# Kernel optimization log

Hardware: AMD Instinct MI355X
Metric: run time of the kernel (lower is better)

## Reference

```python
import jax, jax.numpy as jnp
import numpy as np

B, S, D = 4, 1024, 1024
H, DH = 16, 64
F = 4 * D
EPS = 1e-6


def _ln(x, scale, bias, axes=-1):
    mean = jnp.mean(x, axis=axes, keepdims=True)
    var = jnp.var(x, axis=axes, keepdims=True)
    return (x - mean) * jax.lax.rsqrt(var + EPS) * scale + bias


def setup_inputs() -> dict:
    key = jax.random.key(0)
    ks = jax.random.split(key, 20)
    sd = 1.0 / np.sqrt(D)
    sf = 1.0 / np.sqrt(F)
    inp = {
        'x': jax.random.normal(ks[0], (B, S, D), jnp.float32),
        'z': jax.random.normal(ks[1], (B, S, D), jnp.float32),
        'ln1_s': jnp.ones((D,), jnp.float32),
        'ln1_b': jnp.zeros((D,), jnp.float32),
        'Wq': jax.random.normal(ks[2], (D, D), jnp.float32) * sd,
        'bq': jnp.zeros((D,), jnp.float32),
        'Wk': jax.random.normal(ks[3], (D, D), jnp.float32) * sd,
        'bk': jnp.zeros((D,), jnp.float32),
        'Wv': jax.random.normal(ks[4], (D, D), jnp.float32) * sd,
        'bv': jnp.zeros((D,), jnp.float32),
        'qn_s': jnp.ones((H, DH), jnp.float32),
        'qn_b': jnp.zeros((H, DH), jnp.float32),
        'kn_s': jnp.ones((H, DH), jnp.float32),
        'kn_b': jnp.zeros((H, DH), jnp.float32),
        'Wo': jax.random.normal(ks[5], (D, D), jnp.float32) * sd,
        'bo': jnp.zeros((D,), jnp.float32),
        'ln2_s': jnp.ones((D,), jnp.float32),
        'ln2_b': jnp.zeros((D,), jnp.float32),
        'W1': jax.random.normal(ks[6], (D, F), jnp.float32) * sd,
        'b1': jnp.zeros((F,), jnp.float32),
        'W2': jax.random.normal(ks[7], (D, F), jnp.float32) * sd,
        'b2': jnp.zeros((F,), jnp.float32),
        'W3': jax.random.normal(ks[8], (F, D), jnp.float32) * sf,
        'b3': jnp.zeros((D,), jnp.float32),
    }
    return inp


def reference(x, z, ln1_s, ln1_b, Wq, bq, Wk, bk, Wv, bv, qn_s, qn_b, kn_s, kn_b,
              Wo, bo, ln2_s, ln2_b, W1, b1, W2, b2, W3, b3):
    # z is unused by the original module body
    x_skip = x
    xn = _ln(x, ln1_s, ln1_b)
    q = (xn @ Wq + bq).reshape(B, S, H, DH)
    k = (xn @ Wk + bk).reshape(B, S, H, DH)
    v = (xn @ Wv + bv).reshape(B, S, H, DH)
    # QK-norm: flax LayerNorm(feature_axes=(-2,-1)) still reduces over axis -1,
    # but carries (H, DH)-shaped scale/bias
    q = _ln(q, qn_s, qn_b)
    k = _ln(k, kn_s, kn_b)
    attn = jnp.einsum('bqhd,bkhd->bhqk', q, k) / jnp.sqrt(jnp.asarray(DH, q.dtype))
    attn = jax.nn.softmax(attn, axis=-1)
    out = jnp.einsum('bhqk,bkhd->bqhd', attn, v).reshape(B, S, D)
    x = x_skip + out @ Wo + bo
    x_skip = x
    xn = _ln(x, ln2_s, ln2_b)
    x1 = xn @ W1 + b1
    x2 = xn @ W2 + b2
    h = x1 * jax.nn.gelu(x2, approximate=True)  # GeGLU
    x = x_skip + h @ W3 + b3
    return x
```

## Files before the change

kernel.cpp:

```cpp
#include <hip/hip_runtime.h>

typedef unsigned short u16;
typedef __bf16  bfrag  __attribute__((ext_vector_type(8)));
typedef float   f32x4  __attribute__((ext_vector_type(4)));
typedef u16     u16x8  __attribute__((ext_vector_type(8)));
typedef u16     u16x4  __attribute__((ext_vector_type(4)));

__device__ __forceinline__ float bf2f(u16 u) {
    unsigned v = ((unsigned)u) << 16;
    return __builtin_bit_cast(float, v);
}
__device__ __forceinline__ u16 f2bf(float f) {
    unsigned x = __builtin_bit_cast(unsigned, f);
    unsigned r = (x + 0x7fffu + ((x >> 16) & 1u)) >> 16;
    return (u16)r;
}
__device__ __forceinline__ void g2l16(const u16* g, u16* l) {
    __builtin_amdgcn_global_load_lds((__attribute__((address_space(1))) void*)g,
                                     (__attribute__((address_space(3))) void*)l, 16, 0, 0);
}
__device__ __forceinline__ float gelu_tanh(float x) {
    float c = 1.5957691216057308f * (x + 0.044715f * x * x * x);
    return x * __frcp_rn(1.0f + __expf(-c));
}

#define SW64(l)   (((((l) & 7) ^ (((l) >> 3) & 7))) * 8)
#define RS64(kk, quad, l15)  (((((kk) * 4 + (quad)) ^ ((l15) & 7))) * 8)

__global__ __launch_bounds__(256) void wtln(
        const float* __restrict__ Wq, const float* __restrict__ Wk,
        const float* __restrict__ Wv, const float* __restrict__ Wo,
        const float* __restrict__ W1, const float* __restrict__ W2,
        const float* __restrict__ W3,
        u16* __restrict__ WqkvT, u16* __restrict__ WoT,
        u16* __restrict__ W12T, u16* __restrict__ W3T,
        const float* __restrict__ x, const float* __restrict__ ln1_s,
        const float* __restrict__ ln1_b, u16* __restrict__ xn1) {
    __shared__ float tile[32][33];
    int blk = blockIdx.x;
    if (blk >= 16384) {
        int row = blk - 16384, t = threadIdx.x;
        float4 v = ((const float4*)(x + (size_t)row * 1024))[t];
        float sum = v.x + v.y + v.z + v.w;
        float sq  = v.x * v.x + v.y * v.y + v.z * v.z + v.w * v.w;
#pragma unroll
        for (int off = 1; off < 64; off <<= 1) {
            sum += __shfl_xor(sum, off);
            sq  += __shfl_xor(sq,  off);
        }
        float* s1 = &tile[0][0];
        float* s2 = &tile[0][8];
        int wave = t >> 6;
        if ((t & 63) == 0) { s1[wave] = sum; s2[wave] = sq; }
        __syncthreads();
        sum = s1[0] + s1[1] + s1[2] + s1[3];
        sq  = s2[0] + s2[1] + s2[2] + s2[3];
        float mean = sum * (1.0f / 1024.0f);
        float var  = sq  * (1.0f / 1024.0f) - mean * mean;
        float inv  = rsqrtf(var + 1e-6f);
        float4 sc = ((const float4*)ln1_s)[t], bb = ((const float4*)ln1_b)[t];
        u16x4 o;
        o[0] = f2bf((v.x - mean) * inv * sc.x + bb.x);
        o[1] = f2bf((v.y - mean) * inv * sc.y + bb.y);
        o[2] = f2bf((v.z - mean) * inv * sc.z + bb.z);
        o[3] = f2bf((v.w - mean) * inv * sc.w + bb.w);
        *(u16x4*)&xn1[(size_t)row * 1024 + t * 4] = o;
        return;
    }
    const float* W; u16* Wt; int R, C, local; int ilv = -1;
    if (blk < 3072) {
        int w = blk >> 10; local = blk & 1023;
        W = (w == 0) ? Wq : (w == 1) ? Wk : Wv;
        Wt = WqkvT + (size_t)w * 1024 * 1024; R = 1024; C = 1024;
    } else if (blk < 4096) { W = Wo; Wt = WoT; R = 1024; C = 1024; local = blk - 3072; }
    else if (blk < 8192)   { W = W1; Wt = W12T; R = 1024; C = 4096; local = blk - 4096; ilv = 0; }
    else if (blk < 12288)  { W = W2; Wt = W12T; R = 1024; C = 4096; local = blk - 8192; ilv = 1; }
    else                   { W = W3; Wt = W3T; R = 4096; C = 1024; local = blk - 12288; }
    int tiles_x = C >> 5;
    int c0 = (local % tiles_x) * 32, r0 = (local / tiles_x) * 32;
    int tx = threadIdx.x & 31, ty = threadIdx.x >> 5;
#pragma unroll
    for (int i = 0; i < 32; i += 8)
        tile[ty + i][tx] = W[(size_t)(r0 + ty + i) * C + c0 + tx];
    __syncthreads();
#pragma unroll
    for (int i = 0; i < 32; i += 8) {
        int c = c0 + ty + i;
        int orow = (ilv < 0) ? c : ((c >> 6) * 128 + ilv * 64 + (c & 63));
        Wt[(size_t)orow * R + r0 + tx] = f2bf(tile[tx][ty + i]);
    }
}

template <int EPI>
__global__ __launch_bounds__(256, 3) void gemm64(const u16* __restrict__ A,
                                                 const u16* __restrict__ Bt,
                                                 const float* __restrict__ bias,
                                                 const float* __restrict__ bias2,
                                                 const float* __restrict__ bias3,
                                                 const float* __restrict__ qn_s,
                                                 const float* __restrict__ qn_b,
                                                 const float* __restrict__ kn_s,
                                                 const float* __restrict__ kn_b,
                                                 u16* __restrict__ o0,
                                                 u16* __restrict__ o1,
                                                 u16* __restrict__ o2,
                                                 u16* __restrict__ o3,
                                                 int M, int N, int K, int Klen) {
    __shared__ u16 As[128 * 64];
    __shared__ u16 Bs[128 * 64];
    int tid = threadIdx.x, wave = tid >> 6, lane = tid & 63;
    int quad = lane >> 4, l15 = lane & 15;
    int row0 = blockIdx.y * 128, col0 = blockIdx.x * 128;
    int kz = blockIdx.z;
    int wr = (wave >> 1) * 64, wc = (wave & 1) * 64;
    int swz = SW64(lane);

    f32x4 acc[4][4] = {};

    const u16* gA = A  + (size_t)(row0 + wave * 32 + (lane >> 3)) * K + kz * Klen + swz;
    const u16* gB = Bt + (size_t)(col0 + wave * 32 + (lane >> 3)) * K + kz * Klen + swz;
    u16* lA = &As[wave * 32 * 64];
    u16* lB = &Bs[wave * 32 * 64];

    for (int k0 = 0; k0 < Klen; k0 += 64) {
        __syncthreads();
#pragma unroll
        for (int j = 0; j < 4; j++) {
            g2l16(gA + k0 + j * 8 * K, lA + j * 8 * 64);
            g2l16(gB + k0 + j * 8 * K, lB + j * 8 * 64);
        }
        __syncthreads();
#pragma unroll
        for (int kk = 0; kk < 2; kk++) {
            int rs = RS64(kk, quad, l15);
            bfrag af[4], bf[4];
#pragma unroll
            for (int mi = 0; mi < 4; mi++)
                af[mi] = *(const bfrag*)&As[(wr + mi * 16 + l15) * 64 + rs];
#pragma unroll
            for (int ni = 0; ni < 4; ni++)
                bf[ni] = *(const bfrag*)&Bs[(wc + ni * 16 + l15) * 64 + rs];
#pragma unroll
            for (int mi = 0; mi < 4; mi++)
#pragma unroll
                for (int ni = 0; ni < 4; ni++)
                    acc[mi][ni] = __builtin_amdgcn_mfma_f32_16x16x32_bf16(
                        af[mi], bf[ni], acc[mi][ni], 0, 0, 0);
        }
    }

    if (EPI == 0) {
        u16* P = (kz == 0) ? o0 : (kz == 1) ? o1 : (kz == 2) ? o2 : o3;
#pragma unroll
        for (int mi = 0; mi < 4; mi++) {
            int rbase = row0 + wr + mi * 16 + quad * 4;
#pragma unroll
            for (int r = 0; r < 4; r++)
#pragma unroll
                for (int ni = 0; ni < 4; ni++)
                    P[(size_t)(rbase + r) * N + col0 + wc + ni * 16 + l15] =
                        f2bf(acc[mi][ni][r]);
        }
    } else {
        int cbase = col0 + wc;
        int z = cbase >> 10;
        int hd = (cbase >> 6) & 15;
        const float* bp = (z == 0) ? bias : (z == 1) ? bias2 : bias3;
        float post = (z == 0) ? 0.125f : 1.0f;
        float bv[4], sn[4], bn[4];
#pragma unroll
        for (int ni = 0; ni < 4; ni++)
            bv[ni] = bp[(cbase & 1023) + ni * 16 + l15];
        if (z < 2) {
            const float* ns = (z == 0) ? qn_s : kn_s;
            const float* nb = (z == 0) ? qn_b : kn_b;
#pragma unroll
            for (int ni = 0; ni < 4; ni++) {
                sn[ni] = ns[hd * 64 + ni * 16 + l15];
                bn[ni] = nb[hd * 64 + ni * 16 + l15];
            }
        }
#pragma unroll
        for (int mi = 0; mi < 4; mi++) {
            int rbase = row0 + wr + mi * 16 + quad * 4;
#pragma unroll
            for (int r = 0; r < 4; r++) {
                float v0 = acc[mi][0][r] + bv[0];
                float v1 = acc[mi][1][r] + bv[1];
                float v2 = acc[mi][2][r] + bv[2];
                float v3 = acc[mi][3][r] + bv[3];
                size_t rb = (size_t)(rbase + r) * N + cbase;
                if (z == 2) {
                    o0[rb + 0 * 16 + l15] = f2bf(v0);
                    o0[rb + 1 * 16 + l15] = f2bf(v1);
                    o0[rb + 2 * 16 + l15] = f2bf(v2);
                    o0[rb + 3 * 16 + l15] = f2bf(v3);
                } else {
                    float s  = v0 + v1 + v2 + v3;
                    float sq = v0 * v0 + v1 * v1 + v2 * v2 + v3 * v3;
#pragma unroll
                    for (int m = 1; m < 16; m <<= 1) {
                        s  += __shfl_xor(s,  m);
                        sq += __shfl_xor(sq, m);
                    }
                    float mean = s * (1.0f / 64.0f);
                    float var  = sq * (1.0f / 64.0f) - mean * mean;
                    float inv  = rsqrtf(var + 1e-6f);
                    o0[rb + 0 * 16 + l15] = f2bf(((v0 - mean) * inv * sn[0] + bn[0]) * post);
                    o0[rb + 1 * 16 + l15] = f2bf(((v1 - mean) * inv * sn[1] + bn[1]) * post);
                    o0[rb + 2 * 16 + l15] = f2bf(((v2 - mean) * inv * sn[2] + bn[2]) * post);
                    o0[rb + 3 * 16 + l15] = f2bf(((v3 - mean) * inv * sn[3] + bn[3]) * post);
                }
            }
        }
    }
}

#define PH8(BUFI, S, ISSUE, TAIL)                                              \
  {                                                                            \
    const u16* LA = sm + (BUFI) * 32768;                                       \
    const u16* LB = LA + 16384;                                                \
    if ((S) == 0) {                                                            \
      _Pragma("unroll") for (int ni = 0; ni < 4; ++ni)                         \
      _Pragma("unroll") for (int kk = 0; kk < 2; ++kk)                         \
        bfr[ni][kk] = *(const bfrag*)&LB[(wcg + ni * 16 + l15) * 64            \
                                         + RS64(kk, quad, l15)];               \
    }                                                                          \
    bfrag a00 = *(const bfrag*)&LA[(wr128 + ((S)*2)     * 16 + l15) * 64 + RS64(0, quad, l15)]; \
    bfrag a01 = *(const bfrag*)&LA[(wr128 + ((S)*2)     * 16 + l15) * 64 + RS64(1, quad, l15)]; \
    bfrag a10 = *(const bfrag*)&LA[(wr128 + ((S)*2 + 1) * 16 + l15) * 64 + RS64(0, quad, l15)]; \
    bfrag a11 = *(const bfrag*)&LA[(wr128 + ((S)*2 + 1) * 16 + l15) * 64 + RS64(1, quad, l15)]; \
    ISSUE;                                                                     \
    asm volatile("" ::: "memory");                                             \
    __builtin_amdgcn_s_barrier();                                              \
    asm volatile("s_waitcnt lgkmcnt(0)" ::: "memory");                         \
    __builtin_amdgcn_s_setprio(1);                                             \
    _Pragma("unroll") for (int ni = 0; ni < 4; ++ni) {                         \
      acc[(S)*2][ni]     = __builtin_amdgcn_mfma_f32_16x16x32_bf16(a00, bfr[ni][0], acc[(S)*2][ni], 0, 0, 0);         \
      acc[(S)*2][ni]     = __builtin_amdgcn_mfma_f32_16x16x32_bf16(a01, bfr[ni][1], acc[(S)*2][ni], 0, 0, 0);         \
      acc[(S)*2 + 1][ni] = __builtin_amdgcn_mfma_f32_16x16x32_bf16(a10, bfr[ni][0], acc[(S)*2 + 1][ni], 0, 0, 0);     \
      acc[(S)*2 + 1][ni] = __builtin_amdgcn_mfma_f32_16x16x32_bf16(a11, bfr[ni][1], acc[(S)*2 + 1][ni], 0, 0, 0);     \
    }                                                                          \
    __builtin_amdgcn_s_setprio(0);                                             \
    TAIL;                                                                      \
    asm volatile("" ::: "memory");                                             \
    __builtin_amdgcn_s_barrier();                                              \
    asm volatile("" ::: "memory");                                             \
  }

__global__ __launch_bounds__(512, 2) void gemm_w12_8ph(
        const u16* __restrict__ A, const u16* __restrict__ BI,
        const float* __restrict__ b1, const float* __restrict__ b2,
        u16* __restrict__ H) {
    extern __shared__ __align__(16) u16 sm[];
    int tid = threadIdx.x, w = tid >> 6, lane = tid & 63;
    int quad = lane >> 4, l15 = lane & 15;
    int row0  = blockIdx.y * 256;
    int nrow0 = blockIdx.x * 256;
    int wr128 = (w >> 2) * 128, wcg = (w & 3) * 64;
    int strow = w * 8 + (lane >> 3);
    int swz8  = ((lane & 7) ^ ((lane >> 3) & 7)) * 8;
    int lw8   = w * 8;

    const u16* gA = A  + (size_t)(row0  + strow) * 1024 + swz8;
    const u16* gB = BI + (size_t)(nrow0 + strow) * 1024 + swz8;

    f32x4 acc[8][4] = {};
    bfrag bfr[4][2];

    auto stage = [&](int bufi, int isB, int half, int t) {
        const u16* g = (isB ? gB : gA) + (size_t)half * 128 * 1024 + t * 64;
        u16* l = sm + bufi * 32768 + isB * 16384 + (half * 128 + lw8) * 64;
        g2l16(g, l);
        g2l16(g + 64 * 1024, l + 64 * 64);
    };

    stage(0, 1, 0, 0); stage(0, 1, 1, 0);
    stage(0, 0, 0, 0); stage(0, 0, 1, 0);
    stage(1, 1, 0, 1); stage(1, 1, 1, 1);
    asm volatile("s_waitcnt vmcnt(4)" ::: "memory");
    __builtin_amdgcn_s_barrier();
    asm volatile("" ::: "memory");

#pragma unroll 1
    for (int i = 0; i < 8; ++i) {
        int t = 2 * i;
        bool more = (i < 7);
        PH8(0, 0, { stage(1, 0, 0, t + 1); }, {});
        PH8(0, 1, { stage(1, 0, 1, t + 1); }, {});
        PH8(0, 2, { if (more) stage(0, 1, 0, t + 2); }, {});
        PH8(0, 3, { if (more) stage(0, 1, 1, t + 2); },
                  { if (more) asm volatile("s_waitcnt vmcnt(4)" ::: "memory");
                    else      asm volatile("s_waitcnt vmcnt(0)" ::: "memory"); });
        PH8(1, 0, { if (more) stage(0, 0, 0, t + 2); }, {});
        PH8(1, 1, { if (more) stage(0, 0, 1, t + 2); }, {});
        PH8(1, 2, { if (more) stage(1, 1, 0, t + 3); }, {});
        PH8(1, 3, { if (more) stage(1, 1, 1, t + 3); },
                  { if (more) asm volatile("s_waitcnt vmcnt(4)" ::: "memory"); });
    }

    int c0 = blockIdx.x * 128 + ((w & 3) >> 1) * 64;
    const float* bp = (w & 1) ? b2 : b1;
    float bvv[4];
#pragma unroll
    for (int ni = 0; ni < 4; ++ni) bvv[ni] = bp[c0 + ni * 16 + l15];

    float* xg = (float*)(void*)sm + (w >> 1) * (128 * 64);
    if (w & 1) {
#pragma unroll
        for (int mi = 0; mi < 8; ++mi)
#pragma unroll
        for (int ni = 0; ni < 4; ++ni) {
            int lc = (ni * 16 + l15) ^ (quad << 4);
#pragma unroll
            for (int r = 0; r < 4; ++r)
                xg[(mi * 16 + quad * 4 + r) * 64 + lc] =
                    gelu_tanh(acc[mi][ni][r] + bvv[ni]);
        }
    }
    asm volatile("" ::: "memory");
    __builtin_amdgcn_s_barrier();
    asm volatile("" ::: "memory");
    if (!(w & 1)) {
#pragma unroll
        for (int mi = 0; mi < 8; ++mi) {
            int gr = row0 + wr128 + mi * 16 + quad * 4;
#pragma unroll
            for (int r = 0; r < 4; ++r)
#pragma unroll
            for (int ni = 0; ni < 4; ++ni) {
                float g = xg[(mi * 16 + quad * 4 + r) * 64
                             + ((ni * 16 + l15) ^ (quad << 4))];
                H[(size_t)(gr + r) * 4096 + c0 + ni * 16 + l15] =
                    f2bf((acc[mi][ni][r] + bvv[ni]) * g);
            }
        }
    }
}

__global__ __launch_bounds__(256) void reduce_ln(const u16* __restrict__ p0,
                                                 const u16* __restrict__ p1,
                                                 const float* __restrict__ x,
                                                 const float* __restrict__ bo,
                                                 const float* __restrict__ s,
                                                 const float* __restrict__ b,
                                                 float* __restrict__ xmid,
                                                 u16* __restrict__ xn2) {
    int row = blockIdx.x, t = threadIdx.x;
    size_t i = (size_t)row * 1024 + t * 4;
    float4 xv = *(const float4*)&x[i];
    float4 bb = *(const float4*)&bo[t * 4];
    u16x4 a0 = *(const u16x4*)&p0[i];
    u16x4 a1 = *(const u16x4*)&p1[i];
    float4 v;
    v.x = xv.x + bb.x + bf2f(a0[0]) + bf2f(a1[0]);
    v.y = xv.y + bb.y + bf2f(a0[1]) + bf2f(a1[1]);
    v.z = xv.z + bb.z + bf2f(a0[2]) + bf2f(a1[2]);
    v.w = xv.w + bb.w + bf2f(a0[3]) + bf2f(a1[3]);
    *(float4*)&xmid[i] = v;
    float sum = v.x + v.y + v.z + v.w;
    float sq  = v.x * v.x + v.y * v.y + v.z * v.z + v.w * v.w;
#pragma unroll
    for (int off = 1; off < 64; off <<= 1) {
        sum += __shfl_xor(sum, off);
        sq  += __shfl_xor(sq,  off);
    }
    __shared__ float s1[4], s2[4];
    int wave = t >> 6;
    if ((t & 63) == 0) { s1[wave] = sum; s2[wave] = sq; }
    __syncthreads();
    sum = s1[0] + s1[1] + s1[2] + s1[3];
    sq  = s2[0] + s2[1] + s2[2] + s2[3];
    float mean = sum * (1.0f / 1024.0f);
    float var  = sq  * (1.0f / 1024.0f) - mean * mean;
    float inv  = rsqrtf(var + 1e-6f);
    float4 sc = ((const float4*)s)[t], lb = ((const float4*)b)[t];
    u16x4 o;
    o[0] = f2bf((v.x - mean) * inv * sc.x + lb.x);
    o[1] = f2bf((v.y - mean) * inv * sc.y + lb.y);
    o[2] = f2bf((v.z - mean) * inv * sc.z + lb.z);
    o[3] = f2bf((v.w - mean) * inv * sc.w + lb.w);
    *(u16x4*)&xn2[i] = o;
}

__global__ __launch_bounds__(256) void reduce4(const u16* __restrict__ p0,
                                               const u16* __restrict__ p1,
                                               const u16* __restrict__ p2,
                                               const u16* __restrict__ p3,
                                               const float* __restrict__ xmid,
                                               const float* __restrict__ b3,
                                               float* __restrict__ out) {
    size_t i = ((size_t)blockIdx.x * 256 + threadIdx.x) * 4;
    float4 xm = *(const float4*)&xmid[i];
    float4 bb = *(const float4*)&b3[i & 1023];
    u16x4 a0 = *(const u16x4*)&p0[i];
    u16x4 a1 = *(const u16x4*)&p1[i];
    u16x4 a2 = *(const u16x4*)&p2[i];
    u16x4 a3 = *(const u16x4*)&p3[i];
    float4 o;
    o.x = xm.x + bb.x + bf2f(a0[0]) + bf2f(a1[0]) + bf2f(a2[0]) + bf2f(a3[0]);
    o.y = xm.y + bb.y + bf2f(a0[1]) + bf2f(a1[1]) + bf2f(a2[1]) + bf2f(a3[1]);
    o.z = xm.z + bb.z + bf2f(a0[2]) + bf2f(a1[2]) + bf2f(a2[2]) + bf2f(a3[2]);
    o.w = xm.w + bb.w + bf2f(a0[3]) + bf2f(a1[3]) + bf2f(a2[3]) + bf2f(a3[3]);
    *(float4*)&out[i] = o;
}

#define LPK 72
#define LPV 72
#define LPP 68
__global__ __launch_bounds__(256, 4) void flash(const u16* __restrict__ qkv,
                                                u16* __restrict__ o) {
    int qt = blockIdx.x, h = blockIdx.y, b = blockIdx.z;
    int tid = threadIdx.x, wave = tid >> 6, lane = tid & 63;
    int quad = lane >> 4, l15 = lane & 15;

    __shared__ u16 Ks[64 * LPK];
    __shared__ u16 Vt[64 * LPV];
    __shared__ u16 Ps[64 * LPP];

    const u16* qrow = qkv + (size_t)(b * 1024 + qt * 64 + wave * 16 + l15) * 3072
                      + h * 64 + quad * 8;
    bfrag aq0 = *(const bfrag*)qrow;
    bfrag aq1 = *(const bfrag*)(qrow + 32);

    f32x4 accO[4] = {};
    float l_run[4] = {0.f, 0.f, 0.f, 0.f};

    for (int kt = 0; kt < 16; kt++) {
        __syncthreads();
        {
            int row = tid >> 2, seg = tid & 3;
            const u16* ksrc = qkv + (size_t)(b * 1024 + kt * 64 + row) * 3072
                              + 1024 + h * 64 + seg * 16;
            *(u16x8*)&Ks[row * LPK + seg * 16]     = *(const u16x8*)ksrc;
            *(u16x8*)&Ks[row * LPK + seg * 16 + 8] = *(const u16x8*)(ksrc + 8);
        }
        {
            const u16* vsrc = qkv + (size_t)(b * 1024 + kt * 64 + lane) * 3072
                              + 2048 + h * 64 + wave * 16;
            u16x8 v0 = *(const u16x8*)vsrc, v1 = *(const u16x8*)(vsrc + 8);
#pragma unroll
            for (int j = 0; j < 8; j++) Vt[(wave * 16 + j) * LPV + lane]     = v0[j];
#pragma unroll
            for (int j = 0; j < 8; j++) Vt[(wave * 16 + 8 + j) * LPV + lane] = v1[j];
        }
        __syncthreads();

        f32x4 accS[4] = {};
#pragma unroll
        for (int ct = 0; ct < 4; ct++) {
            bfrag bk0 = *(const bfrag*)&Ks[(ct * 16 + l15) * LPK + quad * 8];
            bfrag bk1 = *(const bfrag*)&Ks[(ct * 16 + l15) * LPK + 32 + quad * 8];
            accS[ct] = __builtin_amdgcn_mfma_f32_16x16x32_bf16(aq0, bk0, accS[ct], 0, 0, 0);
            accS[ct] = __builtin_amdgcn_mfma_f32_16x16x32_bf16(aq1, bk1, accS[ct], 0, 0, 0);
        }

#pragma unroll
        for (int r = 0; r < 4; r++) {
            float p0 = __expf(accS[0][r]);
            float p1 = __expf(accS[1][r]);
            float p2 = __expf(accS[2][r]);
            float p3 = __expf(accS[3][r]);
            l_run[r] += (p0 + p1) + (p2 + p3);
            int pbase = (wave * 16 + quad * 4 + r) * LPP + l15;
            Ps[pbase + 0]  = f2bf(p0);
            Ps[pbase + 16] = f2bf(p1);
            Ps[pbase + 32] = f2bf(p2);
            Ps[pbase + 48] = f2bf(p3);
        }

#pragma unroll
        for (int kk = 0; kk < 2; kk++) {
            const u16* pp = &Ps[(wave * 16 + l15) * LPP + kk * 32 + quad * 8];
            u16x4 lo = *(const u16x4*)pp;
            u16x4 hi = *(const u16x4*)(pp + 4);
            u16x8 apu;
            apu[0] = lo[0]; apu[1] = lo[1]; apu[2] = lo[2]; apu[3] = lo[3];
            apu[4] = hi[0]; apu[5] = hi[1]; apu[6] = hi[2]; apu[7] = hi[3];
            bfrag ap = __builtin_bit_cast(bfrag, apu);
#pragma unroll
            for (int oc = 0; oc < 4; oc++) {
                bfrag bv = *(const bfrag*)&Vt[(oc * 16 + l15) * LPV + kk * 32 + quad * 8];
                accO[oc] = __builtin_amdgcn_mfma_f32_16x16x32_bf16(ap, bv, accO[oc], 0, 0, 0);
            }
        }
    }

#pragma unroll
    for (int r = 0; r < 4; r++) {
        float l = l_run[r];
#pragma unroll
        for (int m = 1; m < 16; m <<= 1) l += __shfl_xor(l, m);
        float linv = 1.0f / l;
        int srow = qt * 64 + wave * 16 + quad * 4 + r;
#pragma unroll
        for (int oc = 0; oc < 4; oc++)
            o[(size_t)(b * 1024 + srow) * 1024 + h * 64 + oc * 16 + l15] =
                f2bf(accO[oc][r] * linv);
    }
}

extern "C" void kernel_launch(void* const* d_in, const int* in_sizes, int n_in,
                              void* d_out, int out_size, void* d_ws, size_t ws_size,
                              hipStream_t stream) {
    const float* x     = (const float*)d_in[0];
    const float* ln1_s = (const float*)d_in[2];
    const float* ln1_b = (const float*)d_in[3];
    const float* Wq = (const float*)d_in[4];  const float* bq = (const float*)d_in[5];
    const float* Wk = (const float*)d_in[6];  const float* bk = (const float*)d_in[7];
    const float* Wv = (const float*)d_in[8];  const float* bv = (const float*)d_in[9];
    const float* qn_s = (const float*)d_in[10]; const float* qn_b = (const float*)d_in[11];
    const float* kn_s = (const float*)d_in[12]; const float* kn_b = (const float*)d_in[13];
    const float* Wo = (const float*)d_in[14]; const float* bo = (const float*)d_in[15];
    const float* ln2_s = (const float*)d_in[16]; const float* ln2_b = (const float*)d_in[17];
    const float* W1 = (const float*)d_in[18]; const float* b1 = (const float*)d_in[19];
    const float* W2 = (const float*)d_in[20]; const float* b2 = (const float*)d_in[21];
    const float* W3 = (const float*)d_in[22]; const float* b3 = (const float*)d_in[23];
    float* out = (float*)d_out;

    char* ws = (char*)d_ws;
    const size_t MB = (size_t)1 << 20;
    u16* WqkvT = (u16*)(ws + 0);
    u16* WoT   = (u16*)(ws + 6 * MB);
    u16* W12T  = (u16*)(ws + 8 * MB);
    u16* W3T   = (u16*)(ws + 24 * MB);
    u16* xn1   = (u16*)(ws + 32 * MB);
    u16* attn  = (u16*)(ws + 32 * MB);
    u16* xn2   = (u16*)(ws + 32 * MB);
    u16* qkv   = (u16*)(ws + 40 * MB);
    float* xmid = (float*)(ws + 40 * MB);
    u16* p3    = (u16*)(ws + 56 * MB);
    u16* h     = (u16*)(ws + 64 * MB);
    u16* wp0   = (u16*)(ws + 64 * MB);
    u16* wp1   = (u16*)(ws + 72 * MB);
    u16* p0    = (u16*)(ws + 0);
    u16* p1    = (u16*)(ws + 8 * MB);
    u16* p2    = (u16*)(ws + 16 * MB);

    wtln<<<20480, 256, 0, stream>>>(Wq, Wk, Wv, Wo, W1, W2, W3,
                                    WqkvT, WoT, W12T, W3T,
                                    x, ln1_s, ln1_b, xn1);

    gemm64<4><<<dim3(24, 32, 1), 256, 0, stream>>>(
        xn1, WqkvT, bq, bk, bv, qn_s, qn_b, kn_s, kn_b,
        qkv, nullptr, nullptr, nullptr, 4096, 3072, 1024, 1024);

    flash<<<dim3(16, 16, 4), 256, 0, stream>>>(qkv, attn);

    gemm64<0><<<dim3(8, 32, 2), 256, 0, stream>>>(
        attn, WoT, nullptr, nullptr, nullptr, nullptr, nullptr, nullptr, nullptr,
        wp0, wp1, nullptr, nullptr, 4096, 1024, 1024, 512);

    reduce_ln<<<4096, 256, 0, stream>>>(wp0, wp1, x, bo, ln2_s, ln2_b, xmid, xn2);

    gemm_w12_8ph<<<dim3(32, 16), 512, 131072, stream>>>(xn2, W12T, b1, b2, h);

    gemm64<0><<<dim3(8, 32, 4), 256, 0, stream>>>(
        h, W3T, nullptr, nullptr, nullptr, nullptr, nullptr, nullptr, nullptr,
        p0, p1, p2, p3, 4096, 1024, 4096, 1024);

    reduce4<<<4096, 256, 0, stream>>>(p0, p1, p2, p3, xmid, b3, out);
}
```

Measured before the change: 417.6 us.

## Remap W12 GEMM block order for XCD locality and split staging per phase

The W1/W2 GeGLU GEMM now launches as a 1D grid and remaps block ids so each group of consecutive blocks (one per XCD round-robin slot) covers neighbouring output tiles, aiming to improve L2 reuse of A and B panels. The global-to-LDS staging is reorganized so A rows for each wave come from its own compute quadrant and loads are issued in finer per-phase chunks, with waitcnts placed mid-iteration. This lets compute start on a partially loaded buffer and spreads memory issue more evenly across phases, but depends on the vmcnt accounting being exact.

```diff
diff --git a/kernel.cpp b/kernel.cpp
--- a/kernel.cpp
+++ b/kernel.cpp
@@ -215,6 +215,8 @@
         }
     }
 }
+
+#define VMC(n)  asm volatile("s_waitcnt vmcnt(" #n ")" ::: "memory")
 
 #define PH8(BUFI, S, ISSUE, TAIL)                                              \
   {                                                                            \
@@ -255,51 +257,62 @@
     extern __shared__ __align__(16) u16 sm[];
     int tid = threadIdx.x, w = tid >> 6, lane = tid & 63;
     int quad = lane >> 4, l15 = lane & 15;
-    int row0  = blockIdx.y * 256;
-    int nrow0 = blockIdx.x * 256;
+
+    int raw  = blockIdx.x;
+    int orig = (raw & 7) * 64 + (raw >> 3);
+    int bx = orig >> 4, by = orig & 15;
+    int row0  = by * 256;
+    int nrow0 = bx * 256;
+
     int wr128 = (w >> 2) * 128, wcg = (w & 3) * 64;
-    int strow = w * 8 + (lane >> 3);
     int swz8  = ((lane & 7) ^ ((lane >> 3) & 7)) * 8;
-    int lw8   = w * 8;
-
-    const u16* gA = A  + (size_t)(row0  + strow) * 1024 + swz8;
-    const u16* gB = BI + (size_t)(nrow0 + strow) * 1024 + swz8;
+
+    int rA = (w >> 2) * 128 + (w & 3) * 8 + (lane >> 3);
+    const u16* gA2 = A + (size_t)(row0 + rA) * 1024 + swz8;
+    int aRowW = (w >> 2) * 128 + (w & 3) * 8;
+    int rB = w * 8 + (lane >> 3);
+    const u16* gB2 = BI + (size_t)(nrow0 + rB) * 1024 + swz8;
+    int bRowW = w * 8;
 
     f32x4 acc[8][4] = {};
     bfrag bfr[4][2];
 
-    auto stage = [&](int bufi, int isB, int half, int t) {
-        const u16* g = (isB ? gB : gA) + (size_t)half * 128 * 1024 + t * 64;
-        u16* l = sm + bufi * 32768 + isB * 16384 + (half * 128 + lw8) * 64;
-        g2l16(g, l);
-        g2l16(g + 64 * 1024, l + 64 * 64);
+    auto stageA = [&](int bufi, int s, int t) {
+        g2l16(gA2 + (size_t)s * 32 * 1024 + t * 64,
+              sm + bufi * 32768 + (aRowW + s * 32) * 64);
     };
-
-    stage(0, 1, 0, 0); stage(0, 1, 1, 0);
-    stage(0, 0, 0, 0); stage(0, 0, 1, 0);
-    stage(1, 1, 0, 1); stage(1, 1, 1, 1);
-    asm volatile("s_waitcnt vmcnt(4)" ::: "memory");
+    auto stageB = [&](int bufi, int b, int t) {
+        g2l16(gB2 + (size_t)b * 64 * 1024 + t * 64,
+              sm + bufi * 32768 + 16384 + (bRowW + b * 64) * 64);
+    };
+
+    stageB(0, 0, 0); stageB(0, 1, 0); stageB(0, 2, 0); stageB(0, 3, 0);
+    stageA(0, 0, 0); stageA(0, 1, 0); stageA(0, 2, 0); stageA(0, 3, 0);
+    stageB(1, 0, 1); stageB(1, 1, 1); stageB(1, 2, 1); stageB(1, 3, 1);
+    stageA(1, 0, 1); stageA(1, 1, 1);
+    VMC(8);
     __builtin_amdgcn_s_barrier();
     asm volatile("" ::: "memory");
 
 #pragma unroll 1
     for (int i = 0; i < 8; ++i) {
-        int t = 2 * i;
+        int t1 = 2 * i + 1, t2 = 2 * i + 2, t3 = 2 * i + 3;
         bool more = (i < 7);
-        PH8(0, 0, { stage(1, 0, 0, t + 1); }, {});
-        PH8(0, 1, { stage(1, 0, 1, t + 1); }, {});
-        PH8(0, 2, { if (more) stage(0, 1, 0, t + 2); }, {});
-        PH8(0, 3, { if (more) stage(0, 1, 1, t + 2); },
-                  { if (more) asm volatile("s_waitcnt vmcnt(4)" ::: "memory");
-                    else      asm volatile("s_waitcnt vmcnt(0)" ::: "memory"); });
-        PH8(1, 0, { if (more) stage(0, 0, 0, t + 2); }, {});
-        PH8(1, 1, { if (more) stage(0, 0, 1, t + 2); }, {});
-        PH8(1, 2, { if (more) stage(1, 1, 0, t + 3); }, {});
-        PH8(1, 3, { if (more) stage(1, 1, 1, t + 3); },
-                  { if (more) asm volatile("s_waitcnt vmcnt(4)" ::: "memory"); });
-    }
-
-    int c0 = blockIdx.x * 128 + ((w & 3) >> 1) * 64;
+        PH8(0, 0, { stageA(1, 2, t1); stageA(1, 3, t1); }, {});
+        PH8(0, 1, { if (more) { stageB(0, 0, t2); stageB(0, 1, t2); } },
+                  { if (more) VMC(10); else VMC(8); });
+        PH8(0, 2, { if (more) { stageB(0, 2, t2); stageB(0, 3, t2); } }, {});
+        PH8(0, 3, { if (more) { stageA(0, 0, t2); stageA(0, 1, t2); } },
+                  { if (more) VMC(8); else VMC(2); });
+        PH8(1, 0, { if (more) { stageA(0, 2, t2); stageA(0, 3, t2); } }, {});
+        PH8(1, 1, { if (more) { stageB(1, 0, t3); stageB(1, 1, t3); } },
+                  { if (more) VMC(10); else VMC(0); });
+        PH8(1, 2, { if (more) { stageB(1, 2, t3); stageB(1, 3, t3); } }, {});
+        PH8(1, 3, { if (more) { stageA(1, 0, t3); stageA(1, 1, t3); } },
+                  { if (more) VMC(8); });
+    }
+
+    int c0 = bx * 128 + ((w & 3) >> 1) * 64;
     const float* bp = (w & 1) ? b2 : b1;
     float bvv[4];
 #pragma unroll
@@ -553,7 +566,7 @@
 
     reduce_ln<<<4096, 256, 0, stream>>>(wp0, wp1, x, bo, ln2_s, ln2_b, xmid, xn2);
 
-    gemm_w12_8ph<<<dim3(32, 16), 512, 131072, stream>>>(xn2, W12T, b1, b2, h);
+    gemm_w12_8ph<<<dim3(512, 1), 512, 131072, stream>>>(xn2, W12T, b1, b2, h);
 
     gemm64<0><<<dim3(8, 32, 4), 256, 0, stream>>>(
         h, W3T, nullptr, nullptr, nullptr, nullptr, nullptr, nullptr, nullptr,
```

Measured after the change: 414.6 us. Within noise of the previous version (-0.7%).
